# Kernel optimization log

Hardware: AMD Instinct MI355X
Metric: run time of the kernel (lower is better)

The kernel has to match this reference:

```python
import jax, jax.numpy as jnp
import numpy as np

B, N, D = 8, 4096, 512


def setup_inputs() -> dict:
    key = jax.random.key(0)
    k1, k2 = jax.random.split(key)
    tgt = jax.random.normal(k1, (B, N, D), dtype=jnp.float32)
    query_pos = jax.random.normal(k2, (B, N, D), dtype=jnp.float32)
    objects_num = N  # scalar int, unused by the math (as in the torch module)
    return {"tgt": tgt, "query_pos": query_pos, "objects_num": objects_num}


def reference(tgt, query_pos, objects_num):
    # L2-normalize along feature dim (torch .norm default: 2-norm, no eps)
    tgt_norm = tgt / jnp.linalg.norm(tgt, axis=-1, keepdims=True)
    # cosine similarity matrix [B, N, N]
    sim = jnp.einsum("bnd,bmd->bnm", tgt_norm, tgt_norm)
    # elementwise tanh, then re-aggregate original (un-normalized) tgt
    out = jnp.einsum("bnm,bmd->bnd", jnp.tanh(sim), tgt)
    return out
```

## Files before the change

kernel.cpp:

```cpp
#include <hip/hip_runtime.h>
#include <hip/hip_bf16.h>

#define B_ 8
#define N_ 4096
#define D_ 512
#define BM 128
#define BK 64
#define NTH 512
#define NT (N_ / BK)

typedef __attribute__((ext_vector_type(8))) short bf16x8;
typedef __attribute__((ext_vector_type(4))) float f32x4;
typedef __attribute__((ext_vector_type(16))) float f32x16;

__device__ __forceinline__ short f2bs(float x) {
  union { __hip_bfloat16 h; short s; } u;
  u.h = __float2bfloat16(x);
  return u.s;
}

__device__ __forceinline__ void gld16(const void* g, void* l) {
  __builtin_amdgcn_global_load_lds((const __attribute__((address_space(1))) void*)g,
                                   (__attribute__((address_space(3))) void*)l, 16, 0, 0);
}

__global__ void __launch_bounds__(256) prep_kernel(const float* __restrict__ tgt,
                                                   ushort* __restrict__ Tbf2,
                                                   ushort* __restrict__ Vt2) {
  __shared__ ushort L[32][520];
  const int id = blockIdx.x;
  const int b = id >> 7, rg = id & 127;
  const int n0 = rg * 32;
  const int t = threadIdx.x;
  const int r = t >> 3, q = t & 7;

  const float* src = tgt + ((size_t)b * N_ + n0 + r) * D_;
  ushort* T2 = Tbf2 + (size_t)b * N_ * D_;
  ushort* V2 = Vt2  + (size_t)b * N_ * D_;

  float4 f[8][2];
  float ss = 0.0f;
  #pragma unroll
  for (int c = 0; c < 8; ++c) {
    const float* p = src + (c * 8 + q) * 8;
    f[c][0] = *(const float4*)p;
    f[c][1] = *(const float4*)(p + 4);
    ss += f[c][0].x * f[c][0].x + f[c][0].y * f[c][0].y
        + f[c][0].z * f[c][0].z + f[c][0].w * f[c][0].w
        + f[c][1].x * f[c][1].x + f[c][1].y * f[c][1].y
        + f[c][1].z * f[c][1].z + f[c][1].w * f[c][1].w;
  }
  ss += __shfl_xor(ss, 1, 64);
  ss += __shfl_xor(ss, 2, 64);
  ss += __shfl_xor(ss, 4, 64);
  const float rs = rsqrtf(ss);

  #pragma unroll
  for (int c = 0; c < 8; ++c) {
    const int g2 = c * 8 + q;
    bf16x8 nv, rv;
    nv[0]=f2bs(f[c][0].x*rs); nv[1]=f2bs(f[c][0].y*rs);
    nv[2]=f2bs(f[c][0].z*rs); nv[3]=f2bs(f[c][0].w*rs);
    nv[4]=f2bs(f[c][1].x*rs); nv[5]=f2bs(f[c][1].y*rs);
    nv[6]=f2bs(f[c][1].z*rs); nv[7]=f2bs(f[c][1].w*rs);
    *(bf16x8*)(T2 + ((size_t)g2 * N_ + n0 + r) * 8) = nv;
    rv[0]=f2bs(f[c][0].x); rv[1]=f2bs(f[c][0].y);
    rv[2]=f2bs(f[c][0].z); rv[3]=f2bs(f[c][0].w);
    rv[4]=f2bs(f[c][1].x); rv[5]=f2bs(f[c][1].y);
    rv[6]=f2bs(f[c][1].z); rv[7]=f2bs(f[c][1].w);
    #pragma unroll
    for (int e = 0; e < 8; ++e) L[r][g2 * 8 + e] = (ushort)rv[e];
  }
  __syncthreads();

  #pragma unroll
  for (int c2 = 0; c2 < 8; ++c2) {
    int tau = c2 * 256 + t;
    int ng = tau >> 9, d = tau & 511;
    bf16x8 v;
    #pragma unroll
    for (int j = 0; j < 8; ++j) v[j] = (short)L[ng * 8 + j][d];
    *(bf16x8*)(V2 + ((size_t)(n0 / 8 + ng) * D_ + d) * 8) = v;
  }
}

__global__ void __launch_bounds__(NTH, 2) fused_kernel(const ushort* __restrict__ Tbf2,
                                                       const ushort* __restrict__ Vt2,
                                                       float* __restrict__ out) {
  __shared__ __align__(16) ushort KV[BK * D_];
  __shared__ __align__(16) ushort VT[BK * D_];
  __shared__ __align__(16) ushort Pl[BM * BK];

  const int id = blockIdx.x;
  const int b  = id & 7;
  const int q0 = (id >> 3) * BM;

  const int lane = threadIdx.x & 63;
  const int w    = threadIdx.x >> 6;
  const int qG   = w;

  const ushort* Tb2 = Tbf2 + (size_t)b * N_ * D_;
  const ushort* Vb2 = Vt2  + (size_t)b * N_ * D_;

  bf16x8 qf[16];
  {
    const int row = q0 + qG * 16 + (lane & 15);
    #pragma unroll
    for (int kk = 0; kk < 16; ++kk) {
      int g = kk * 4 + (lane >> 4);
      qf[kk] = *(const bf16x8*)(Tb2 + ((size_t)g * N_ + row) * 8);
    }
  }

  f32x16 acc[4][2] = {};

  const ushort* kvrd = &KV[(lane >> 4) * 512 + (lane & 15) * 8];
  const ushort* pard = &Pl[(lane >> 5) * 1024 + (lane & 31) * 8];
  const ushort* vbrd = &VT[(lane >> 5) * 4096 + (w * 64 + (lane & 31)) * 8];
  ushort*       plwr = &Pl[((lane & 15) >> 3) * 1024
                           + (qG * 16 + (lane >> 4) * 4) * 8
                           + (lane & 7)];

  const ushort* kvsrc = Tb2 + (size_t)(w * 8) * N_ * 8 + (size_t)BK * 8 + lane * 8;
  const ushort* vtsrc = Vb2 + (size_t)(8 + w) * D_ * 8 + lane * 8;

  #pragma unroll
  for (int i = 0; i < 8; ++i)
    gld16(Tb2 + ((size_t)(w * 8 + i) * N_) * 8 + lane * 8, &KV[(w * 8 + i) * 512]);
  #pragma unroll
  for (int i = 0; i < 8; ++i)
    gld16(Vb2 + (size_t)w * D_ * 8 + i * 512 + lane * 8, &VT[w * 4096 + i * 512]);
  __syncthreads();

  for (int t = 0; t < NT; ++t) {
    f32x4 sacc[4] = {};
    __builtin_amdgcn_s_setprio(1);
    #pragma unroll
    for (int kk = 0; kk < 16; ++kk) {
      #pragma unroll
      for (int f = 0; f < 4; ++f) {
        bf16x8 bf = *(const bf16x8*)(kvrd + kk * 2048 + f * 128);
        sacc[f] = __builtin_amdgcn_mfma_f32_16x16x32_bf16(qf[kk], bf, sacc[f], 0, 0, 0);
      }
    }
    __builtin_amdgcn_s_setprio(0);

    #pragma unroll
    for (int f = 0; f < 4; ++f)
      #pragma unroll
      for (int j = 0; j < 4; ++j) {
        float e = __builtin_amdgcn_exp2f(sacc[f][j] * 2.885390082f);
        float tn = 1.0f - 2.0f * __builtin_amdgcn_rcpf(e + 1.0f);
        plwr[f * 2048 + j * 8] = (ushort)f2bs(tn);
      }
    __syncthreads();

    if (t < NT - 1) {
      #pragma unroll
      for (int i = 0; i < 8; ++i)
        gld16(kvsrc + (size_t)i * N_ * 8, &KV[(w * 8 + i) * 512]);
      kvsrc += BK * 8;
    }

    __builtin_amdgcn_s_setprio(1);
    #pragma unroll
    for (int ks = 0; ks < 4; ++ks) {
      bf16x8 vb0 = *(const bf16x8*)(vbrd + ks * 8192);
      bf16x8 vb1 = *(const bf16x8*)(vbrd + ks * 8192 + 256);
      #pragma unroll
      for (int qb = 0; qb < 4; ++qb) {
        bf16x8 pa = *(const bf16x8*)(pard + ks * 2048 + qb * 256);
        acc[qb][0] = __builtin_amdgcn_mfma_f32_32x32x16_bf16(pa, vb0, acc[qb][0], 0, 0, 0);
        acc[qb][1] = __builtin_amdgcn_mfma_f32_32x32x16_bf16(pa, vb1, acc[qb][1], 0, 0, 0);
      }
    }
    __builtin_amdgcn_s_setprio(0);
    __syncthreads();

    if (t < NT - 1) {
      #pragma unroll
      for (int i = 0; i < 8; ++i)
        gld16(vtsrc + i * 512, &VT[w * 4096 + i * 512]);
      vtsrc += 8 * D_ * 8;
    }
  }

  {
    float* op = out + (size_t)b * N_ * D_ + (size_t)q0 * D_;
    #pragma unroll
    for (int qb = 0; qb < 4; ++qb)
      #pragma unroll
      for (int ds = 0; ds < 2; ++ds) {
        int d = w * 64 + ds * 32 + (lane & 31);
        #pragma unroll
        for (int reg = 0; reg < 16; ++reg) {
          int row = qb * 32 + (reg & 3) + 8 * (reg >> 2) + 4 * (lane >> 5);
          op[(size_t)row * D_ + d] = acc[qb][ds][reg];
        }
      }
  }
}

extern "C" void kernel_launch(void* const* d_in, const int* in_sizes, int n_in,
                              void* d_out, int out_size, void* d_ws, size_t ws_size,
                              hipStream_t stream) {
  const float* tgt = (const float*)d_in[0];
  float* outp = (float*)d_out;

  ushort* Tbf2 = (ushort*)d_ws;
  ushort* Vt2  = Tbf2 + (size_t)B_ * N_ * D_;

  prep_kernel<<<dim3(B_ * 128), dim3(256), 0, stream>>>(tgt, Tbf2, Vt2);
  fused_kernel<<<dim3(B_ * (N_ / BM)), dim3(NTH), 0, stream>>>(Tbf2, Vt2, outp);
}
```

Measured before the change: 280.3 us.

## Double-buffer K tiles in LDS and load V fragments directly into registers

```diff
diff --git a/kernel.cpp b/kernel.cpp
--- a/kernel.cpp
+++ b/kernel.cpp
@@ -87,8 +87,7 @@
 __global__ void __launch_bounds__(NTH, 2) fused_kernel(const ushort* __restrict__ Tbf2,
                                                        const ushort* __restrict__ Vt2,
                                                        float* __restrict__ out) {
-  __shared__ __align__(16) ushort KV[BK * D_];
-  __shared__ __align__(16) ushort VT[BK * D_];
+  __shared__ __align__(16) ushort KV[2][BK * D_];
   __shared__ __align__(16) ushort Pl[BM * BK];
 
   const int id = blockIdx.x;
@@ -114,25 +113,42 @@
 
   f32x16 acc[4][2] = {};
 
-  const ushort* kvrd = &KV[(lane >> 4) * 512 + (lane & 15) * 8];
-  const ushort* pard = &Pl[(lane >> 5) * 1024 + (lane & 31) * 8];
-  const ushort* vbrd = &VT[(lane >> 5) * 4096 + (w * 64 + (lane & 31)) * 8];
-  ushort*       plwr = &Pl[((lane & 15) >> 3) * 1024
-                           + (qG * 16 + (lane >> 4) * 4) * 8
-                           + (lane & 7)];
+  const int kvo = (lane >> 4) * 512 + (lane & 15) * 8;
+  const ushort* kvrd0 = &KV[0][kvo];
+  const ushort* kvrd1 = &KV[1][kvo];
+  const ushort* pard  = &Pl[(lane >> 5) * 1024 + (lane & 31) * 8];
+  ushort*       plwr  = &Pl[((lane & 15) >> 3) * 1024
+                            + (qG * 16 + (lane >> 4) * 4) * 8
+                            + (lane & 7)];
+  ushort* kvst0 = &KV[0][w * 8 * 512];
+  ushort* kvst1 = &KV[1][w * 8 * 512];
 
   const ushort* kvsrc = Tb2 + (size_t)(w * 8) * N_ * 8 + (size_t)BK * 8 + lane * 8;
-  const ushort* vtsrc = Vb2 + (size_t)(8 + w) * D_ * 8 + lane * 8;
+  const ushort* vbase = Vb2 + ((size_t)(lane >> 5) * D_ + w * 64 + (lane & 31)) * 8;
 
   #pragma unroll
   for (int i = 0; i < 8; ++i)
-    gld16(Tb2 + ((size_t)(w * 8 + i) * N_) * 8 + lane * 8, &KV[(w * 8 + i) * 512]);
-  #pragma unroll
-  for (int i = 0; i < 8; ++i)
-    gld16(Vb2 + (size_t)w * D_ * 8 + i * 512 + lane * 8, &VT[w * 4096 + i * 512]);
+    gld16(Tb2 + ((size_t)(w * 8 + i) * N_) * 8 + lane * 8, kvst0 + i * 512);
   __syncthreads();
 
   for (int t = 0; t < NT; ++t) {
+    if (t < NT - 1) {
+      ushort* kvst = ((t + 1) & 1) ? kvst1 : kvst0;
+      #pragma unroll
+      for (int i = 0; i < 8; ++i)
+        gld16(kvsrc + (size_t)i * N_ * 8, kvst + i * 512);
+      kvsrc += BK * 8;
+    }
+
+    bf16x8 vr[4][2];
+    #pragma unroll
+    for (int ks = 0; ks < 4; ++ks) {
+      vr[ks][0] = *(const bf16x8*)(vbase + (size_t)ks * 2 * D_ * 8);
+      vr[ks][1] = *(const bf16x8*)(vbase + (size_t)ks * 2 * D_ * 8 + 256);
+    }
+    vbase += (size_t)8 * D_ * 8;
+
+    const ushort* kvrd = (t & 1) ? kvrd1 : kvrd0;
     f32x4 sacc[4] = {};
     __builtin_amdgcn_s_setprio(1);
     #pragma unroll
@@ -155,34 +171,18 @@
       }
     __syncthreads();
 
-    if (t < NT - 1) {
-      #pragma unroll
-      for (int i = 0; i < 8; ++i)
-        gld16(kvsrc + (size_t)i * N_ * 8, &KV[(w * 8 + i) * 512]);
-      kvsrc += BK * 8;
-    }
-
     __builtin_amdgcn_s_setprio(1);
     #pragma unroll
     for (int ks = 0; ks < 4; ++ks) {
-      bf16x8 vb0 = *(const bf16x8*)(vbrd + ks * 8192);
-      bf16x8 vb1 = *(const bf16x8*)(vbrd + ks * 8192 + 256);
       #pragma unroll
       for (int qb = 0; qb < 4; ++qb) {
         bf16x8 pa = *(const bf16x8*)(pard + ks * 2048 + qb * 256);
-        acc[qb][0] = __builtin_amdgcn_mfma_f32_32x32x16_bf16(pa, vb0, acc[qb][0], 0, 0, 0);
-        acc[qb][1] = __builtin_amdgcn_mfma_f32_32x32x16_bf16(pa, vb1, acc[qb][1], 0, 0, 0);
+        acc[qb][0] = __builtin_amdgcn_mfma_f32_32x32x16_bf16(pa, vr[ks][0], acc[qb][0], 0, 0, 0);
+        acc[qb][1] = __builtin_amdgcn_mfma_f32_32x32x16_bf16(pa, vr[ks][1], acc[qb][1], 0, 0, 0);
       }
     }
     __builtin_amdgcn_s_setprio(0);
     __syncthreads();
-
-    if (t < NT - 1) {
-      #pragma unroll
-      for (int i = 0; i < 8; ++i)
-        gld16(vtsrc + i * 512, &VT[w * 4096 + i * 512]);
-      vtsrc += 8 * D_ * 8;
-    }
   }
 
   {
```

New measurement: 313.2 us. 1.12x slower.

## Split QK^T reduction across wave pairs with bf16 partial sums in LDS

Applied to the files above, without the earlier changes.

```diff
diff --git a/kernel.cpp b/kernel.cpp
--- a/kernel.cpp
+++ b/kernel.cpp
@@ -17,6 +17,11 @@
   union { __hip_bfloat16 h; short s; } u;
   u.h = __float2bfloat16(x);
   return u.s;
+}
+__device__ __forceinline__ float bs2f(ushort s) {
+  union { unsigned u; float f; } v;
+  v.u = ((unsigned)s) << 16;
+  return v.f;
 }
 
 __device__ __forceinline__ void gld16(const void* g, void* l) {
@@ -90,6 +95,7 @@
   __shared__ __align__(16) ushort KV[BK * D_];
   __shared__ __align__(16) ushort VT[BK * D_];
   __shared__ __align__(16) ushort Pl[BM * BK];
+  __shared__ __align__(16) ushort Pp[BM * BK];
 
   const int id = blockIdx.x;
   const int b  = id & 7;
@@ -97,29 +103,31 @@
 
   const int lane = threadIdx.x & 63;
   const int w    = threadIdx.x >> 6;
-  const int qG   = w;
+  const int ks   = w & 1;
+  const int qG   = w >> 1;
 
   const ushort* Tb2 = Tbf2 + (size_t)b * N_ * D_;
   const ushort* Vb2 = Vt2  + (size_t)b * N_ * D_;
 
-  bf16x8 qf[16];
-  {
-    const int row = q0 + qG * 16 + (lane & 15);
-    #pragma unroll
-    for (int kk = 0; kk < 16; ++kk) {
-      int g = kk * 4 + (lane >> 4);
-      qf[kk] = *(const bf16x8*)(Tb2 + ((size_t)g * N_ + row) * 8);
+  bf16x8 qf[2][8];
+  #pragma unroll
+  for (int qs = 0; qs < 2; ++qs) {
+    const int row = q0 + qG * 32 + qs * 16 + (lane & 15);
+    #pragma unroll
+    for (int kk = 0; kk < 8; ++kk) {
+      int g = ks * 32 + kk * 4 + (lane >> 4);
+      qf[qs][kk] = *(const bf16x8*)(Tb2 + ((size_t)g * N_ + row) * 8);
     }
   }
 
   f32x16 acc[4][2] = {};
 
-  const ushort* kvrd = &KV[(lane >> 4) * 512 + (lane & 15) * 8];
+  const ushort* kvrd = &KV[ks * 16384 + (lane >> 4) * 512 + (lane & 15) * 8];
   const ushort* pard = &Pl[(lane >> 5) * 1024 + (lane & 31) * 8];
-  const ushort* vbrd = &VT[(lane >> 5) * 4096 + (w * 64 + (lane & 31)) * 8];
-  ushort*       plwr = &Pl[((lane & 15) >> 3) * 1024
-                           + (qG * 16 + (lane >> 4) * 4) * 8
-                           + (lane & 7)];
+  const int pidx = ((lane & 15) >> 3) * 1024
+                 + (qG * 32 + (lane >> 4) * 4) * 8 + (lane & 7);
+  ushort* PlW = &Pl[pidx];
+  ushort* PpW = &Pp[pidx];
 
   const ushort* kvsrc = Tb2 + (size_t)(w * 8) * N_ * 8 + (size_t)BK * 8 + lane * 8;
   const ushort* vtsrc = Vb2 + (size_t)(8 + w) * D_ * 8 + lane * 8;
@@ -133,26 +141,40 @@
   __syncthreads();
 
   for (int t = 0; t < NT; ++t) {
-    f32x4 sacc[4] = {};
+    ushort* W = ks ? PpW : PlW;
     __builtin_amdgcn_s_setprio(1);
     #pragma unroll
-    for (int kk = 0; kk < 16; ++kk) {
-      #pragma unroll
-      for (int f = 0; f < 4; ++f) {
+    for (int f = 0; f < 4; ++f) {
+      f32x4 s0 = {}, s1 = {};
+      #pragma unroll
+      for (int kk = 0; kk < 8; ++kk) {
         bf16x8 bf = *(const bf16x8*)(kvrd + kk * 2048 + f * 128);
-        sacc[f] = __builtin_amdgcn_mfma_f32_16x16x32_bf16(qf[kk], bf, sacc[f], 0, 0, 0);
+        s0 = __builtin_amdgcn_mfma_f32_16x16x32_bf16(qf[0][kk], bf, s0, 0, 0, 0);
+        s1 = __builtin_amdgcn_mfma_f32_16x16x32_bf16(qf[1][kk], bf, s1, 0, 0, 0);
+      }
+      #pragma unroll
+      for (int j = 0; j < 4; ++j) {
+        W[f * 2048 + j * 8]       = (ushort)f2bs(s0[j]);
+        W[f * 2048 + 128 + j * 8] = (ushort)f2bs(s1[j]);
       }
     }
     __builtin_amdgcn_s_setprio(0);
-
-    #pragma unroll
-    for (int f = 0; f < 4; ++f)
-      #pragma unroll
-      for (int j = 0; j < 4; ++j) {
-        float e = __builtin_amdgcn_exp2f(sacc[f][j] * 2.885390082f);
-        float tn = 1.0f - 2.0f * __builtin_amdgcn_rcpf(e + 1.0f);
-        plwr[f * 2048 + j * 8] = (ushort)f2bs(tn);
-      }
+    __syncthreads();
+
+    if (ks == 0) {
+      #pragma unroll
+      for (int f = 0; f < 4; ++f)
+        #pragma unroll
+        for (int qs = 0; qs < 2; ++qs)
+          #pragma unroll
+          for (int j = 0; j < 4; ++j) {
+            int o = f * 2048 + qs * 128 + j * 8;
+            float s = bs2f(PlW[o]) + bs2f(PpW[o]);
+            float e = __builtin_amdgcn_exp2f(s * 2.885390082f);
+            float tn = 1.0f - 2.0f * __builtin_amdgcn_rcpf(e + 1.0f);
+            PlW[o] = (ushort)f2bs(tn);
+          }
+    }
     __syncthreads();
 
     if (t < NT - 1) {
@@ -164,12 +186,14 @@
 
     __builtin_amdgcn_s_setprio(1);
     #pragma unroll
-    for (int ks = 0; ks < 4; ++ks) {
-      bf16x8 vb0 = *(const bf16x8*)(vbrd + ks * 8192);
-      bf16x8 vb1 = *(const bf16x8*)(vbrd + ks * 8192 + 256);
+    for (int kq = 0; kq < 4; ++kq) {
+      bf16x8 vb0 = *(const bf16x8*)(&VT[(lane >> 5) * 4096 + (w * 64 + (lane & 31)) * 8]
+                                    + kq * 8192);
+      bf16x8 vb1 = *(const bf16x8*)(&VT[(lane >> 5) * 4096 + (w * 64 + (lane & 31)) * 8]
+                                    + kq * 8192 + 256);
       #pragma unroll
       for (int qb = 0; qb < 4; ++qb) {
-        bf16x8 pa = *(const bf16x8*)(pard + ks * 2048 + qb * 256);
+        bf16x8 pa = *(const bf16x8*)(pard + kq * 2048 + qb * 256);
         acc[qb][0] = __builtin_amdgcn_mfma_f32_32x32x16_bf16(pa, vb0, acc[qb][0], 0, 0, 0);
         acc[qb][1] = __builtin_amdgcn_mfma_f32_32x32x16_bf16(pa, vb1, acc[qb][1], 0, 0, 0);
       }
```

After: 365.5 us. 1.3x slower.
